# Kernel tuning notes

Measured on AMD Instinct MI355X. Metric: run time of the kernel, lower is better.

The kernel has to match this reference:

```python
import jax, jax.numpy as jnp
import numpy as np

G, N, F, H, B, L = 4, 1024, 256, 256, 32, 4


def setup_inputs() -> dict:
    key = jax.random.key(0)
    ks = jax.random.split(key, 8)
    batch_xs = jax.random.normal(ks[0], (G, N, F), dtype=jnp.float32)
    # dense (preprocessed/normalized) adjacency; scale ~1/N keeps activations stable
    batch_as = jax.random.uniform(ks[1], (G, N, N), dtype=jnp.float32) / N
    w_in = jax.random.normal(ks[2], (F, H), dtype=jnp.float32) * 0.05
    b_in = jnp.zeros((H,), dtype=jnp.float32)
    gcn_w = jax.random.normal(ks[3], (L, H, H), dtype=jnp.float32) * 0.05
    gcn_b = jnp.zeros((L, H), dtype=jnp.float32)
    graph_idx = jax.random.randint(ks[4], (B,), 0, G)
    cp_mask = jax.random.randint(ks[5], (B, N), 0, 2).astype(bool)
    return {"batch_xs": batch_xs, "batch_as": batch_as, "w_in": w_in, "b_in": b_in,
            "gcn_w": gcn_w, "gcn_b": gcn_b, "graph_idx": graph_idx, "cp_mask": cp_mask}


def reference(batch_xs, batch_as, w_in, b_in, gcn_w, gcn_b, graph_idx, cp_mask):
    # gather_nd: select per-example graph features and adjacency
    X = batch_xs[graph_idx]          # [B, N, F]
    A = batch_as[graph_idx]          # [B, N, N]
    # GNN input dense layer (relu); dropout is identity at inference
    x = jax.nn.relu(X @ w_in + b_in)  # [B, N, H]
    res = x                           # residual from post-input activations
    # GCNConv stack: act(A @ x @ W + b); relu for all but final tanh layer
    for i in range(L - 1):
        x = jax.nn.relu(jnp.einsum('bnm,bmh->bnh', A, x) @ gcn_w[i] + gcn_b[i])
    x = jnp.tanh(jnp.einsum('bnm,bmh->bnh', A, x) @ gcn_w[L - 1] + gcn_b[L - 1])
    x = x + res
    # ragged boolean_mask + reduce_mean over nodes == masked mean
    m = cp_mask.astype(x.dtype)       # [B, N]
    denom = jnp.maximum(jnp.sum(m, axis=1, keepdims=True), 1.0)
    return jnp.sum(x * m[..., None], axis=1) / denom  # [B, H]
```

## Files before the change

### kernel.cpp

```cpp
#include <hip/hip_runtime.h>
#include <math.h>

#define G 4
#define NN 1024
#define FF 256
#define HH 256
#define BB 32
#define LL 4

typedef __attribute__((ext_vector_type(8))) short short8;
typedef __attribute__((ext_vector_type(8))) unsigned short ushort8;
typedef __attribute__((ext_vector_type(4))) unsigned short ushort4v;
typedef __attribute__((ext_vector_type(4))) float floatx4;

__device__ inline unsigned short f2bf(float f) {
  union { float f; unsigned u; } x; x.f = f;
  unsigned r = x.u + 0x7fffu + ((x.u >> 16) & 1u);
  return (unsigned short)(r >> 16);
}
__device__ inline float bf2f(unsigned short u) {
  union { unsigned u; float f; } x; x.u = (unsigned)u << 16;
  return x.f;
}

__device__ void in_tile(int job, const float* __restrict__ X,
                        const float* __restrict__ w_in,
                        const float* __restrict__ b_in,
                        unsigned short* __restrict__ xbf,
                        unsigned short* __restrict__ h0bf, unsigned short* As,
                        unsigned short* Bs, int t) {
  const int nt_ = job & 3, mt = (job >> 2) & 15, g = job >> 6;
  const int m0 = mt * 64, n0 = nt_ * 64;
  const int lane = t & 63, w = t >> 6;
  const int wm = w & 1, wn = w >> 1;
  const int l16 = lane & 15, quad = lane >> 4;

  floatx4 acc[2][2];
#pragma unroll
  for (int i = 0; i < 2; ++i)
#pragma unroll
    for (int j = 0; j < 2; ++j) acc[i][j] = (floatx4){0.f, 0.f, 0.f, 0.f};

  for (int tt = 0; tt < 4; ++tt) {
    const int kb = tt * 64;
    __syncthreads();
#pragma unroll
    for (int i = 0; i < 2; ++i) {
      const int q = t + i * 256;
      const int row = q >> 3, c8 = q & 7;
      const float* Af =
          X + (long)g * NN * FF + (long)(m0 + row) * FF + kb + c8 * 8;
      float4 f0 = *(const float4*)Af;
      float4 f1 = *(const float4*)(Af + 4);
      ushort8 v;
      v[0] = f2bf(f0.x); v[1] = f2bf(f0.y); v[2] = f2bf(f0.z); v[3] = f2bf(f0.w);
      v[4] = f2bf(f1.x); v[5] = f2bf(f1.y); v[6] = f2bf(f1.z); v[7] = f2bf(f1.w);
      *(ushort8*)&As[row * 72 + c8 * 8] = v;
    }
    {
      const int row = t >> 2;
      const int c0 = (t & 3) * 16;
#pragma unroll
      for (int j = 0; j < 4; ++j) {
        float4 f = *(const float4*)&w_in[(long)(kb + row) * HH + n0 + c0 + j * 4];
        Bs[(c0 + j * 4 + 0) * 72 + row] = f2bf(f.x);
        Bs[(c0 + j * 4 + 1) * 72 + row] = f2bf(f.y);
        Bs[(c0 + j * 4 + 2) * 72 + row] = f2bf(f.z);
        Bs[(c0 + j * 4 + 3) * 72 + row] = f2bf(f.w);
      }
    }
    __syncthreads();
#pragma unroll
    for (int kk = 0; kk < 64; kk += 32) {
      const int ko = kk + quad * 8;
      short8 a0 = *(const short8*)&As[(wm * 32 + l16) * 72 + ko];
      short8 a1 = *(const short8*)&As[(wm * 32 + 16 + l16) * 72 + ko];
      short8 b0 = *(const short8*)&Bs[(wn * 32 + l16) * 72 + ko];
      short8 b1 = *(const short8*)&Bs[(wn * 32 + 16 + l16) * 72 + ko];
      acc[0][0] = __builtin_amdgcn_mfma_f32_16x16x32_bf16(a0, b0, acc[0][0], 0, 0, 0);
      acc[0][1] = __builtin_amdgcn_mfma_f32_16x16x32_bf16(a0, b1, acc[0][1], 0, 0, 0);
      acc[1][0] = __builtin_amdgcn_mfma_f32_16x16x32_bf16(a1, b0, acc[1][0], 0, 0, 0);
      acc[1][1] = __builtin_amdgcn_mfma_f32_16x16x32_bf16(a1, b1, acc[1][1], 0, 0, 0);
    }
  }

#pragma unroll
  for (int i = 0; i < 2; ++i) {
#pragma unroll
    for (int j = 0; j < 2; ++j) {
      const int n = n0 + wn * 32 + j * 16 + l16;
      const int mB = m0 + wm * 32 + i * 16 + quad * 4;
      const float bv = b_in[n];
#pragma unroll
      for (int r = 0; r < 4; ++r) {
        const unsigned short pv = f2bf(fmaxf(acc[i][j][r] + bv, 0.f));
        xbf[(long)g * NN * HH + (long)(mB + r) * HH + n] = pv;
        h0bf[(long)g * NN * HH + (long)(mB + r) * HH + n] = pv;
      }
    }
  }
}

__device__ void mask_job(int b, const void* __restrict__ cp_mask,
                         float* __restrict__ fmask, float* __restrict__ denom,
                         int t) {
  const unsigned char* bytes = (const unsigned char*)cp_mask;
  __shared__ int fmt;
  __shared__ float red[256];
  if (t == 0) {
    int any = 0;
    for (int i = 0; i < 256; ++i)
      if ((i & 3) && bytes[i]) any = 1;
    fmt = any ? 0 : 1;
  }
  __syncthreads();
  float cnt = 0.f;
  for (int n = t; n < NN; n += 256) {
    float v;
    if (fmt)
      v = ((const int*)cp_mask)[b * NN + n] ? 1.f : 0.f;
    else
      v = bytes[b * NN + n] ? 1.f : 0.f;
    fmask[b * NN + n] = v;
    cnt += v;
  }
  red[t] = cnt;
  __syncthreads();
  for (int s = 128; s > 0; s >>= 1) {
    if (t < s) red[t] += red[t + s];
    __syncthreads();
  }
  if (t == 0) denom[b] = fmaxf(red[0], 1.f);
}

__device__ void gw_job(int j, const float* __restrict__ gcn_w,
                       unsigned short* __restrict__ gwT, int t) {
  const int l = j >> 4, r0 = (j & 15) * 16;
  const float* src = gcn_w + (long)l * HH * HH;
  unsigned short* dst = gwT + (long)l * HH * HH;
  unsigned short vv[16];
#pragma unroll
  for (int rr = 0; rr < 16; ++rr) vv[rr] = f2bf(src[(long)(r0 + rr) * HH + t]);
  *(ushort8*)&dst[(long)t * HH + r0] = *(ushort8*)&vv[0];
  *(ushort8*)&dst[(long)t * HH + r0 + 8] = *(ushort8*)&vv[8];
}

__global__ __launch_bounds__(256) void pre_kernel(
    const float* __restrict__ batch_as, unsigned short* __restrict__ Abf,
    const float* __restrict__ batch_xs, const float* __restrict__ w_in,
    const float* __restrict__ b_in, unsigned short* __restrict__ xbf,
    unsigned short* __restrict__ h0bf, const float* __restrict__ gcn_w,
    unsigned short* __restrict__ gwT, const void* __restrict__ cp_mask,
    float* __restrict__ fmask, float* __restrict__ denom,
    float* __restrict__ out) {
  __shared__ __align__(16) unsigned short As[64 * 72];
  __shared__ __align__(16) unsigned short Bs[64 * 72];
  const int b = blockIdx.x, t = threadIdx.x;
  if (b < 1024) {
    const long idx = ((long)b * 256 + t) * 16;
#pragma unroll
    for (int h = 0; h < 2; ++h) {
      float4 f0 = *(const float4*)&batch_as[idx + h * 8];
      float4 f1 = *(const float4*)&batch_as[idx + h * 8 + 4];
      ushort8 v;
      v[0] = f2bf(f0.x); v[1] = f2bf(f0.y); v[2] = f2bf(f0.z); v[3] = f2bf(f0.w);
      v[4] = f2bf(f1.x); v[5] = f2bf(f1.y); v[6] = f2bf(f1.z); v[7] = f2bf(f1.w);
      *(ushort8*)&Abf[idx + h * 8] = v;
    }
  } else if (b < 1280) {
    in_tile(b - 1024, batch_xs, w_in, b_in, xbf, h0bf, As, Bs, t);
  } else if (b < 1344) {
    gw_job(b - 1280, gcn_w, gwT, t);
  } else if (b < 1376) {
    mask_job(b - 1344, cp_mask, fmask, denom, t);
  } else {
    for (int i = 0; i < 32; ++i) out[i * 256 + t] = 0.f;
  }
}

__global__ __launch_bounds__(256) void g1_kernel(
    const unsigned short* __restrict__ xbf,
    const unsigned short* __restrict__ WT,
    unsigned short* __restrict__ yT) {
  __shared__ __align__(16) unsigned short As[64 * 72];
  __shared__ __align__(16) unsigned short Bs[64 * 72];
  const int n0 = blockIdx.x * 64;
  const int m0 = blockIdx.y * 64;
  const int g = blockIdx.z;
  const int t = threadIdx.x;
  const int lane = t & 63, w = t >> 6;
  const int wm = w & 1, wn = w >> 1;
  const int l16 = lane & 15, quad = lane >> 4;

  const unsigned short* Ab = xbf + (long)g * NN * HH;

  ushort8 pa[2], pb[2];
  auto load_tile = [&](int tt) {
    const int kb = tt * 64;
#pragma unroll
    for (int i = 0; i < 2; ++i) {
      const int q = t + i * 256;
      const int row = q >> 3, c8 = q & 7;
      pa[i] = *(const ushort8*)&Ab[(long)(m0 + row) * HH + kb + c8 * 8];
      pb[i] = *(const ushort8*)&WT[(long)(n0 + row) * HH + kb + c8 * 8];
    }
  };
  auto store_tile = [&]() {
#pragma unroll
    for (int i = 0; i < 2; ++i) {
      const int q = t + i * 256;
      const int row = q >> 3, c8 = q & 7;
      *(ushort8*)&As[row * 72 + c8 * 8] = pa[i];
      *(ushort8*)&Bs[row * 72 + c8 * 8] = pb[i];
    }
  };

  floatx4 acc[2][2];
#pragma unroll
  for (int i = 0; i < 2; ++i)
#pragma unroll
    for (int j = 0; j < 2; ++j) acc[i][j] = (floatx4){0.f, 0.f, 0.f, 0.f};

  load_tile(0);
  for (int tt = 0; tt < 4; ++tt) {
    __syncthreads();
    store_tile();
    __syncthreads();
    if (tt + 1 < 4) load_tile(tt + 1);
#pragma unroll
    for (int kk = 0; kk < 64; kk += 32) {
      const int ko = kk + quad * 8;
      short8 a0 = *(const short8*)&As[(wm * 32 + l16) * 72 + ko];
      short8 a1 = *(const short8*)&As[(wm * 32 + 16 + l16) * 72 + ko];
      short8 b0 = *(const short8*)&Bs[(wn * 32 + l16) * 72 + ko];
      short8 b1 = *(const short8*)&Bs[(wn * 32 + 16 + l16) * 72 + ko];
      acc[0][0] = __builtin_amdgcn_mfma_f32_16x16x32_bf16(a0, b0, acc[0][0], 0, 0, 0);
      acc[0][1] = __builtin_amdgcn_mfma_f32_16x16x32_bf16(a0, b1, acc[0][1], 0, 0, 0);
      acc[1][0] = __builtin_amdgcn_mfma_f32_16x16x32_bf16(a1, b0, acc[1][0], 0, 0, 0);
      acc[1][1] = __builtin_amdgcn_mfma_f32_16x16x32_bf16(a1, b1, acc[1][1], 0, 0, 0);
    }
  }

#pragma unroll
  for (int i = 0; i < 2; ++i) {
#pragma unroll
    for (int j = 0; j < 2; ++j) {
      const int n = n0 + wn * 32 + j * 16 + l16;
      const int mB = m0 + wm * 32 + i * 16 + quad * 4;
      ushort4v pv;
#pragma unroll
      for (int r = 0; r < 4; ++r) pv[r] = f2bf(acc[i][j][r]);
      *(ushort4v*)&yT[(long)g * HH * NN + (long)n * NN + mB] = pv;
    }
  }
}

__global__ __launch_bounds__(512) void fused_kernel(
    const unsigned short* __restrict__ Abf,
    const unsigned short* __restrict__ yT, const float* __restrict__ bias,
    const unsigned short* __restrict__ WT, unsigned short* __restrict__ y2T) {
  __shared__ __align__(16) unsigned short As[16 * 136];
  __shared__ __align__(16) unsigned short Bs[256 * 136];
  __shared__ __align__(16) unsigned short Xs[16 * 264];
  const int m0 = blockIdx.x * 16;
  const int g = blockIdx.y;
  const int t = threadIdx.x;
  const int lane = t & 63, w = t >> 6;
  const int l16 = lane & 15, quad = lane >> 4;

  const unsigned short* Ag = Abf + (long)g * NN * NN + (long)m0 * NN;
  const unsigned short* Bg = yT + (long)g * HH * NN;

  ushort8 pb[8], pa;
  auto load_tile = [&](int tt) {
    const int kb = tt * 128;
#pragma unroll
    for (int i = 0; i < 8; ++i) {
      const int q = t + i * 512;
      const int row = q >> 4, c8 = q & 15;
      pb[i] = *(const ushort8*)&Bg[(long)row * NN + kb + c8 * 8];
    }
    if (t < 256) {
      const int row = t >> 4, c8 = t & 15;
      pa = *(const ushort8*)&Ag[(long)row * NN + kb + c8 * 8];
    }
  };
  auto store_tile = [&]() {
#pragma unroll
    for (int i = 0; i < 8; ++i) {
      const int q = t + i * 512;
      const int row = q >> 4, c8 = q & 15;
      *(ushort8*)&Bs[row * 136 + c8 * 8] = pb[i];
    }
    if (t < 256) {
      const int row = t >> 4, c8 = t & 15;
      *(ushort8*)&As[row * 136 + c8 * 8] = pa;
    }
  };

  floatx4 acc[2];
  acc[0] = (floatx4){0.f, 0.f, 0.f, 0.f};
  acc[1] = (floatx4){0.f, 0.f, 0.f, 0.f};

  load_tile(0);
  for (int tt = 0; tt < 8; ++tt) {
    __syncthreads();
    store_tile();
    __syncthreads();
    if (tt + 1 < 8) load_tile(tt + 1);
#pragma unroll
    for (int kk = 0; kk < 128; kk += 32) {
      const int ko = kk + quad * 8;
      short8 a = *(const short8*)&As[l16 * 136 + ko];
      short8 b0 = *(const short8*)&Bs[(w * 32 + l16) * 136 + ko];
      short8 b1 = *(const short8*)&Bs[(w * 32 + 16 + l16) * 136 + ko];
      acc[0] = __builtin_amdgcn_mfma_f32_16x16x32_bf16(a, b0, acc[0], 0, 0, 0);
      acc[1] = __builtin_amdgcn_mfma_f32_16x16x32_bf16(a, b1, acc[1], 0, 0, 0);
    }
  }

  ushort8 pw[8];
  auto loadW = [&](int t2) {
    const int kb = t2 * 128;
#pragma unroll
    for (int i = 0; i < 8; ++i) {
      const int q = t + i * 512;
      const int row = q >> 4, c8 = q & 15;
      pw[i] = *(const ushort8*)&WT[(long)row * HH + kb + c8 * 8];
    }
  };
  loadW(0);

#pragma unroll
  for (int j = 0; j < 2; ++j) {
    const int n = w * 32 + j * 16 + l16;
    const float bv = bias[n];
#pragma unroll
    for (int r = 0; r < 4; ++r)
      Xs[(quad * 4 + r) * 264 + n] = f2bf(fmaxf(acc[j][r] + bv, 0.f));
  }

  floatx4 acc2[2];
  acc2[0] = (floatx4){0.f, 0.f, 0.f, 0.f};
  acc2[1] = (floatx4){0.f, 0.f, 0.f, 0.f};

  for (int t2 = 0; t2 < 2; ++t2) {
    __syncthreads();
#pragma unroll
    for (int i = 0; i < 8; ++i) {
      const int q = t + i * 512;
      const int row = q >> 4, c8 = q & 15;
      *(ushort8*)&Bs[row * 136 + c8 * 8] = pw[i];
    }
    __syncthreads();
    if (t2 == 0) loadW(1);
    const int kb = t2 * 128;
#pragma unroll
    for (int kk = 0; kk < 128; kk += 32) {
      const int ko = kk + quad * 8;
      short8 a = *(const short8*)&Xs[l16 * 264 + kb + ko];
      short8 b0 = *(const short8*)&Bs[(w * 32 + l16) * 136 + ko];
      short8 b1 = *(const short8*)&Bs[(w * 32 + 16 + l16) * 136 + ko];
      acc2[0] = __builtin_amdgcn_mfma_f32_16x16x32_bf16(a, b0, acc2[0], 0, 0, 0);
      acc2[1] = __builtin_amdgcn_mfma_f32_16x16x32_bf16(a, b1, acc2[1], 0, 0, 0);
    }
  }

#pragma unroll
  for (int j = 0; j < 2; ++j) {
    const int n = w * 32 + j * 16 + l16;
    ushort4v pv;
#pragma unroll
    for (int r = 0; r < 4; ++r) pv[r] = f2bf(acc2[j][r]);
    *(ushort4v*)&y2T[(long)g * HH * NN + (long)n * NN + m0 + quad * 4] = pv;
  }
}

template <int ACT>
__global__ __launch_bounds__(256) void g2_kernel(
    const unsigned short* __restrict__ Abf,
    const unsigned short* __restrict__ yT, const float* __restrict__ bias,
    const unsigned short* __restrict__ h0bf, unsigned short* __restrict__ xbf,
    const float* __restrict__ fmask, const float* __restrict__ denom,
    const int* __restrict__ gidx, float* __restrict__ out) {
  __shared__ __align__(16) unsigned short As[32 * 136];
  __shared__ __align__(16) unsigned short Bs[64 * 136];
  const int n0 = blockIdx.x * 64;
  const int m0 = blockIdx.y * 32;
  const int g = blockIdx.z;
  const int t = threadIdx.x;
  const int lane = t & 63, w = t >> 6;
  const int wm = w & 1, wn = w >> 1;
  const int l16 = lane & 15, quad = lane >> 4;

  const unsigned short* Ag = Abf + (long)g * NN * NN + (long)m0 * NN;
  const unsigned short* Bg = yT + (long)g * HH * NN + (long)n0 * NN;

  ushort8 pa[2], pb[4];
  auto load_tile = [&](int tt) {
    const int kb = tt * 128;
#pragma unroll
    for (int i = 0; i < 2; ++i) {
      const int q = t + i * 256;
      const int row = q >> 4, c8 = q & 15;
      pa[i] = *(const ushort8*)&Ag[(long)row * NN + kb + c8 * 8];
    }
#pragma unroll
    for (int i = 0; i < 4; ++i) {
      const int q = t + i * 256;
      const int row = q >> 4, c8 = q & 15;
      pb[i] = *(const ushort8*)&Bg[(long)row * NN + kb + c8 * 8];
    }
  };
  auto store_tile = [&]() {
#pragma unroll
    for (int i = 0; i < 2; ++i) {
      const int q = t + i * 256;
      const int row = q >> 4, c8 = q & 15;
      *(ushort8*)&As[row * 136 + c8 * 8] = pa[i];
    }
#pragma unroll
    for (int i = 0; i < 4; ++i) {
      const int q = t + i * 256;
      const int row = q >> 4, c8 = q & 15;
      *(ushort8*)&Bs[row * 136 + c8 * 8] = pb[i];
    }
  };

  floatx4 acc[2];
  acc[0] = (floatx4){0.f, 0.f, 0.f, 0.f};
  acc[1] = (floatx4){0.f, 0.f, 0.f, 0.f};

  load_tile(0);
  for (int tt = 0; tt < 8; ++tt) {
    __syncthreads();
    store_tile();
    __syncthreads();
    if (tt + 1 < 8) load_tile(tt + 1);
#pragma unroll
    for (int kk = 0; kk < 128; kk += 32) {
      const int ko = kk + quad * 8;
      short8 a = *(const short8*)&As[(wm * 16 + l16) * 136 + ko];
      short8 b0 = *(const short8*)&Bs[(wn * 32 + l16) * 136 + ko];
      short8 b1 = *(const short8*)&Bs[(wn * 32 + 16 + l16) * 136 + ko];
      acc[0] = __builtin_amdgcn_mfma_f32_16x16x32_bf16(a, b0, acc[0], 0, 0, 0);
      acc[1] = __builtin_amdgcn_mfma_f32_16x16x32_bf16(a, b1, acc[1], 0, 0, 0);
    }
  }

  if (ACT == 1) {
#pragma unroll
    for (int j = 0; j < 2; ++j) {
      const int n = n0 + wn * 32 + j * 16 + l16;
      const int mB = m0 + wm * 16 + quad * 4;
      const float bv = bias[n];
#pragma unroll
      for (int r = 0; r < 4; ++r)
        xbf[(long)g * NN * HH + (long)(mB + r) * HH + n] =
            f2bf(fmaxf(acc[j][r] + bv, 0.f));
    }
  } else {
    const int mB0 = m0 + wm * 16 + quad * 4;
    float zv[2][4];
#pragma unroll
    for (int j = 0; j < 2; ++j) {
      const int n = n0 + wn * 32 + j * 16 + l16;
      const float bv = bias[n];
#pragma unroll
      for (int r = 0; r < 4; ++r) {
        const long idx = (long)g * NN * HH + (long)(mB0 + r) * HH + n;
        zv[j][r] = tanhf(acc[j][r] + bv) + bf2f(h0bf[idx]);
      }
    }
    for (int b = 0; b < BB; ++b) {
      if (gidx[b] != g) continue;
      const float invd = 1.f / denom[b];
      float m4[4];
#pragma unroll
      for (int r = 0; r < 4; ++r) m4[r] = fmask[b * NN + mB0 + r];
#pragma unroll
      for (int j = 0; j < 2; ++j) {
        float p = m4[0] * zv[j][0] + m4[1] * zv[j][1] + m4[2] * zv[j][2] +
                  m4[3] * zv[j][3];
        p += __shfl_xor(p, 16);
        p += __shfl_xor(p, 32);
        if (quad == 0) {
          const int n = n0 + wn * 32 + j * 16 + l16;
          atomicAdd(&out[b * HH + n], p * invd);
        }
      }
    }
  }
}

extern "C" void kernel_launch(void* const* d_in, const int* in_sizes, int n_in,
                              void* d_out, int out_size, void* d_ws,
                              size_t ws_size, hipStream_t stream) {
  (void)in_sizes; (void)n_in; (void)out_size; (void)ws_size;
  const float* batch_xs = (const float*)d_in[0];
  const float* batch_as = (const float*)d_in[1];
  const float* w_in = (const float*)d_in[2];
  const float* b_in = (const float*)d_in[3];
  const float* gcn_w = (const float*)d_in[4];
  const float* gcn_b = (const float*)d_in[5];
  const int* graph_idx = (const int*)d_in[6];
  const void* cp_mask = d_in[7];
  float* out = (float*)d_out;

  char* p = (char*)d_ws;
  unsigned short* Abf = (unsigned short*)p;  p += (long)G * NN * NN * 2;
  unsigned short* gwT = (unsigned short*)p;  p += (long)LL * HH * HH * 2;
  unsigned short* xbf = (unsigned short*)p;  p += (long)G * NN * HH * 2;
  unsigned short* h0bf = (unsigned short*)p; p += (long)G * NN * HH * 2;
  unsigned short* yTa = (unsigned short*)p;  p += (long)G * HH * NN * 2;
  unsigned short* yTb = (unsigned short*)p;  p += (long)G * HH * NN * 2;
  float* fmask = (float*)p;                  p += (long)BB * NN * 4;
  float* denom = (float*)p;                  p += BB * 4;

  pre_kernel<<<1377, 256, 0, stream>>>(batch_as, Abf, batch_xs, w_in, b_in,
                                       xbf, h0bf, gcn_w, gwT, cp_mask, fmask,
                                       denom, out);

  g1_kernel<<<dim3(4, 16, G), 256, 0, stream>>>(xbf, gwT, yTa);

  fused_kernel<<<dim3(64, G), 512, 0, stream>>>(
      Abf, yTa, gcn_b + 0 * HH, gwT + (long)1 * HH * HH, yTb);
  fused_kernel<<<dim3(64, G), 512, 0, stream>>>(
      Abf, yTb, gcn_b + 1 * HH, gwT + (long)2 * HH * HH, yTa);
  fused_kernel<<<dim3(64, G), 512, 0, stream>>>(
      Abf, yTa, gcn_b + 2 * HH, gwT + (long)3 * HH * HH, yTb);

  g2_kernel<0><<<dim3(4, 32, G), 256, 0, stream>>>(
      Abf, yTb, gcn_b + (long)3 * HH, h0bf, nullptr, fmask, denom,
      graph_idx, out);
}
```

Before: 149.5 us.

## Fuse fp32-to-bf16 adjacency conversion into first GCN layer kernel

The separate pass in pre_kernel that converts the fp32 adjacency to bf16 is removed. The first layer kernel now reads the fp32 adjacency directly, converts it while staging into shared memory, and writes the bf16 copy out for later layers. This saves one full read of the bf16 adjacency plus a pass over the data, and shrinks pre_kernel. The K tile is halved from 128 to 64, giving smaller shared-memory tiles but twice as many synchronisation steps. It also drops the duplicate xbf buffer in favour of h0bf, and merges the output zeroing into the mask jobs.

```diff
diff --git a/kernel.cpp b/kernel.cpp
--- a/kernel.cpp
+++ b/kernel.cpp
@@ -26,7 +26,6 @@
 __device__ void in_tile(int job, const float* __restrict__ X,
                         const float* __restrict__ w_in,
                         const float* __restrict__ b_in,
-                        unsigned short* __restrict__ xbf,
                         unsigned short* __restrict__ h0bf, unsigned short* As,
                         unsigned short* Bs, int t) {
   const int nt_ = job & 3, mt = (job >> 2) & 15, g = job >> 6;
@@ -94,7 +93,6 @@
 #pragma unroll
       for (int r = 0; r < 4; ++r) {
         const unsigned short pv = f2bf(fmaxf(acc[i][j][r] + bv, 0.f));
-        xbf[(long)g * NN * HH + (long)(mB + r) * HH + n] = pv;
         h0bf[(long)g * NN * HH + (long)(mB + r) * HH + n] = pv;
       }
     }
@@ -146,35 +144,22 @@
 }
 
 __global__ __launch_bounds__(256) void pre_kernel(
-    const float* __restrict__ batch_as, unsigned short* __restrict__ Abf,
     const float* __restrict__ batch_xs, const float* __restrict__ w_in,
-    const float* __restrict__ b_in, unsigned short* __restrict__ xbf,
-    unsigned short* __restrict__ h0bf, const float* __restrict__ gcn_w,
-    unsigned short* __restrict__ gwT, const void* __restrict__ cp_mask,
-    float* __restrict__ fmask, float* __restrict__ denom,
-    float* __restrict__ out) {
+    const float* __restrict__ b_in, unsigned short* __restrict__ h0bf,
+    const float* __restrict__ gcn_w, unsigned short* __restrict__ gwT,
+    const void* __restrict__ cp_mask, float* __restrict__ fmask,
+    float* __restrict__ denom, float* __restrict__ out) {
   __shared__ __align__(16) unsigned short As[64 * 72];
   __shared__ __align__(16) unsigned short Bs[64 * 72];
   const int b = blockIdx.x, t = threadIdx.x;
-  if (b < 1024) {
-    const long idx = ((long)b * 256 + t) * 16;
-#pragma unroll
-    for (int h = 0; h < 2; ++h) {
-      float4 f0 = *(const float4*)&batch_as[idx + h * 8];
-      float4 f1 = *(const float4*)&batch_as[idx + h * 8 + 4];
-      ushort8 v;
-      v[0] = f2bf(f0.x); v[1] = f2bf(f0.y); v[2] = f2bf(f0.z); v[3] = f2bf(f0.w);
-      v[4] = f2bf(f1.x); v[5] = f2bf(f1.y); v[6] = f2bf(f1.z); v[7] = f2bf(f1.w);
-      *(ushort8*)&Abf[idx + h * 8] = v;
-    }
-  } else if (b < 1280) {
-    in_tile(b - 1024, batch_xs, w_in, b_in, xbf, h0bf, As, Bs, t);
-  } else if (b < 1344) {
-    gw_job(b - 1280, gcn_w, gwT, t);
-  } else if (b < 1376) {
-    mask_job(b - 1344, cp_mask, fmask, denom, t);
+  if (b < 256) {
+    in_tile(b, batch_xs, w_in, b_in, h0bf, As, Bs, t);
+  } else if (b < 320) {
+    gw_job(b - 256, gcn_w, gwT, t);
   } else {
-    for (int i = 0; i < 32; ++i) out[i * 256 + t] = 0.f;
+    const int bb = b - 320;
+    out[bb * HH + t] = 0.f;
+    mask_job(bb, cp_mask, fmask, denom, t);
   }
 }
 
@@ -255,12 +240,15 @@
   }
 }
 
-__global__ __launch_bounds__(512) void fused_kernel(
-    const unsigned short* __restrict__ Abf,
-    const unsigned short* __restrict__ yT, const float* __restrict__ bias,
-    const unsigned short* __restrict__ WT, unsigned short* __restrict__ y2T) {
-  __shared__ __align__(16) unsigned short As[16 * 136];
-  __shared__ __align__(16) unsigned short Bs[256 * 136];
+template <int CONVA>
+__global__ __launch_bounds__(512) void layer_kernel(
+    const float* __restrict__ Af32, const unsigned short* __restrict__ Abf_in,
+    unsigned short* __restrict__ Abf_out,
+    const unsigned short* __restrict__ yT_in, const float* __restrict__ bias,
+    const unsigned short* __restrict__ WT,
+    unsigned short* __restrict__ yT_out) {
+  __shared__ __align__(16) unsigned short As[16 * 72];
+  __shared__ __align__(16) unsigned short Bs[256 * 72];
   __shared__ __align__(16) unsigned short Xs[16 * 264];
   const int m0 = blockIdx.x * 16;
   const int g = blockIdx.y;
@@ -268,33 +256,43 @@
   const int lane = t & 63, w = t >> 6;
   const int l16 = lane & 15, quad = lane >> 4;
 
-  const unsigned short* Ag = Abf + (long)g * NN * NN + (long)m0 * NN;
-  const unsigned short* Bg = yT + (long)g * HH * NN;
-
-  ushort8 pb[8], pa;
+  const unsigned short* Bg = yT_in + (long)g * HH * NN;
+  const int arow = t >> 5, ac2 = t & 31;
+
+  ushort8 pb[4];
+  float2 paF;
+  unsigned int paU;
   auto load_tile = [&](int tt) {
-    const int kb = tt * 128;
-#pragma unroll
-    for (int i = 0; i < 8; ++i) {
+    const int kb = tt * 64;
+#pragma unroll
+    for (int i = 0; i < 4; ++i) {
       const int q = t + i * 512;
-      const int row = q >> 4, c8 = q & 15;
+      const int row = q >> 3, c8 = q & 7;
       pb[i] = *(const ushort8*)&Bg[(long)row * NN + kb + c8 * 8];
     }
-    if (t < 256) {
-      const int row = t >> 4, c8 = t & 15;
-      pa = *(const ushort8*)&Ag[(long)row * NN + kb + c8 * 8];
-    }
-  };
-  auto store_tile = [&]() {
-#pragma unroll
-    for (int i = 0; i < 8; ++i) {
+    if (CONVA) {
+      paF = *(const float2*)&Af32[(long)g * NN * NN + (long)(m0 + arow) * NN +
+                                  kb + ac2 * 2];
+    } else {
+      paU = *(const unsigned int*)&Abf_in[(long)g * NN * NN +
+                                          (long)(m0 + arow) * NN + kb + ac2 * 2];
+    }
+  };
+  auto store_tile = [&](int tt) {
+#pragma unroll
+    for (int i = 0; i < 4; ++i) {
       const int q = t + i * 512;
-      const int row = q >> 4, c8 = q & 15;
-      *(ushort8*)&Bs[row * 136 + c8 * 8] = pb[i];
-    }
-    if (t < 256) {
-      const int row = t >> 4, c8 = t & 15;
-      *(ushort8*)&As[row * 136 + c8 * 8] = pa;
+      const int row = q >> 3, c8 = q & 7;
+      *(ushort8*)&Bs[row * 72 + c8 * 8] = pb[i];
+    }
+    if (CONVA) {
+      const unsigned int packed =
+          (unsigned)f2bf(paF.x) | ((unsigned)f2bf(paF.y) << 16);
+      *(unsigned int*)&As[arow * 72 + ac2 * 2] = packed;
+      *(unsigned int*)&Abf_out[(long)g * NN * NN + (long)(m0 + arow) * NN +
+                               tt * 64 + ac2 * 2] = packed;
+    } else {
+      *(unsigned int*)&As[arow * 72 + ac2 * 2] = paU;
     }
   };
 
@@ -303,29 +301,29 @@
   acc[1] = (floatx4){0.f, 0.f, 0.f, 0.f};
 
   load_tile(0);
-  for (int tt = 0; tt < 8; ++tt) {
-    __syncthreads();
-    store_tile();
-    __syncthreads();
-    if (tt + 1 < 8) load_tile(tt + 1);
-#pragma unroll
-    for (int kk = 0; kk < 128; kk += 32) {
+  for (int tt = 0; tt < 16; ++tt) {
+    __syncthreads();
+    store_tile(tt);
+    __syncthreads();
+    if (tt + 1 < 16) load_tile(tt + 1);
+#pragma unroll
+    for (int kk = 0; kk < 64; kk += 32) {
       const int ko = kk + quad * 8;
-      short8 a = *(const short8*)&As[l16 * 136 + ko];
-      short8 b0 = *(const short8*)&Bs[(w * 32 + l16) * 136 + ko];
-      short8 b1 = *(const short8*)&Bs[(w * 32 + 16 + l16) * 136 + ko];
+      short8 a = *(const short8*)&As[l16 * 72 + ko];
+      short8 b0 = *(const short8*)&Bs[(w * 32 + l16) * 72 + ko];
+      short8 b1 = *(const short8*)&Bs[(w * 32 + 16 + l16) * 72 + ko];
       acc[0] = __builtin_amdgcn_mfma_f32_16x16x32_bf16(a, b0, acc[0], 0, 0, 0);
       acc[1] = __builtin_amdgcn_mfma_f32_16x16x32_bf16(a, b1, acc[1], 0, 0, 0);
     }
   }
 
-  ushort8 pw[8];
+  ushort8 pw[4];
   auto loadW = [&](int t2) {
-    const int kb = t2 * 128;
-#pragma unroll
-    for (int i = 0; i < 8; ++i) {
+    const int kb = t2 * 64;
+#pragma unroll
+    for (int i = 0; i < 4; ++i) {
       const int q = t + i * 512;
-      const int row = q >> 4, c8 = q & 15;
+      const int row = q >> 3, c8 = q & 7;
       pw[i] = *(const ushort8*)&WT[(long)row * HH + kb + c8 * 8];
     }
   };
@@ -344,23 +342,23 @@
   acc2[0] = (floatx4){0.f, 0.f, 0.f, 0.f};
   acc2[1] = (floatx4){0.f, 0.f, 0.f, 0.f};
 
-  for (int t2 = 0; t2 < 2; ++t2) {
-    __syncthreads();
-#pragma unroll
-    for (int i = 0; i < 8; ++i) {
+  for (int t2 = 0; t2 < 4; ++t2) {
+    __syncthreads();
+#pragma unroll
+    for (int i = 0; i < 4; ++i) {
       const int q = t + i * 512;
-      const int row = q >> 4, c8 = q & 15;
-      *(ushort8*)&Bs[row * 136 + c8 * 8] = pw[i];
-    }
-    __syncthreads();
-    if (t2 == 0) loadW(1);
-    const int kb = t2 * 128;
-#pragma unroll
-    for (int kk = 0; kk < 128; kk += 32) {
+      const int row = q >> 3, c8 = q & 7;
+      *(ushort8*)&Bs[row * 72 + c8 * 8] = pw[i];
+    }
+    __syncthreads();
+    if (t2 + 1 < 4) loadW(t2 + 1);
+    const int kb = t2 * 64;
+#pragma unroll
+    for (int kk = 0; kk < 64; kk += 32) {
       const int ko = kk + quad * 8;
       short8 a = *(const short8*)&Xs[l16 * 264 + kb + ko];
-      short8 b0 = *(const short8*)&Bs[(w * 32 + l16) * 136 + ko];
-      short8 b1 = *(const short8*)&Bs[(w * 32 + 16 + l16) * 136 + ko];
+      short8 b0 = *(const short8*)&Bs[(w * 32 + l16) * 72 + ko];
+      short8 b1 = *(const short8*)&Bs[(w * 32 + 16 + l16) * 72 + ko];
       acc2[0] = __builtin_amdgcn_mfma_f32_16x16x32_bf16(a, b0, acc2[0], 0, 0, 0);
       acc2[1] = __builtin_amdgcn_mfma_f32_16x16x32_bf16(a, b1, acc2[1], 0, 0, 0);
     }
@@ -372,7 +370,7 @@
     ushort4v pv;
 #pragma unroll
     for (int r = 0; r < 4; ++r) pv[r] = f2bf(acc2[j][r]);
-    *(ushort4v*)&y2T[(long)g * HH * NN + (long)n * NN + m0 + quad * 4] = pv;
+    *(ushort4v*)&yT_out[(long)g * HH * NN + (long)n * NN + m0 + quad * 4] = pv;
   }
 }
 
@@ -510,25 +508,26 @@
   char* p = (char*)d_ws;
   unsigned short* Abf = (unsigned short*)p;  p += (long)G * NN * NN * 2;
   unsigned short* gwT = (unsigned short*)p;  p += (long)LL * HH * HH * 2;
-  unsigned short* xbf = (unsigned short*)p;  p += (long)G * NN * HH * 2;
   unsigned short* h0bf = (unsigned short*)p; p += (long)G * NN * HH * 2;
   unsigned short* yTa = (unsigned short*)p;  p += (long)G * HH * NN * 2;
   unsigned short* yTb = (unsigned short*)p;  p += (long)G * HH * NN * 2;
   float* fmask = (float*)p;                  p += (long)BB * NN * 4;
   float* denom = (float*)p;                  p += BB * 4;
 
-  pre_kernel<<<1377, 256, 0, stream>>>(batch_as, Abf, batch_xs, w_in, b_in,
-                                       xbf, h0bf, gcn_w, gwT, cp_mask, fmask,
-                                       denom, out);
-
-  g1_kernel<<<dim3(4, 16, G), 256, 0, stream>>>(xbf, gwT, yTa);
-
-  fused_kernel<<<dim3(64, G), 512, 0, stream>>>(
-      Abf, yTa, gcn_b + 0 * HH, gwT + (long)1 * HH * HH, yTb);
-  fused_kernel<<<dim3(64, G), 512, 0, stream>>>(
-      Abf, yTb, gcn_b + 1 * HH, gwT + (long)2 * HH * HH, yTa);
-  fused_kernel<<<dim3(64, G), 512, 0, stream>>>(
-      Abf, yTa, gcn_b + 2 * HH, gwT + (long)3 * HH * HH, yTb);
+  pre_kernel<<<352, 256, 0, stream>>>(batch_xs, w_in, b_in, h0bf, gcn_w, gwT,
+                                      cp_mask, fmask, denom, out);
+
+  g1_kernel<<<dim3(4, 16, G), 256, 0, stream>>>(h0bf, gwT, yTa);
+
+  layer_kernel<1><<<dim3(64, G), 512, 0, stream>>>(
+      batch_as, nullptr, Abf, yTa, gcn_b + 0 * HH, gwT + (long)1 * HH * HH,
+      yTb);
+  layer_kernel<0><<<dim3(64, G), 512, 0, stream>>>(
+      nullptr, Abf, nullptr, yTb, gcn_b + 1 * HH, gwT + (long)2 * HH * HH,
+      yTa);
+  layer_kernel<0><<<dim3(64, G), 512, 0, stream>>>(
+      nullptr, Abf, nullptr, yTa, gcn_b + 2 * HH, gwT + (long)3 * HH * HH,
+      yTb);
 
   g2_kernel<0><<<dim3(4, 32, G), 256, 0, stream>>>(
       Abf, yTb, gcn_b + (long)3 * HH, h0bf, nullptr, fmask, denom,
```

Result: slower. 157.2 us (+5.2%).
